# Kernel tuning notes

Measured on AMD Instinct MI355X. Metric: run time of the kernel, lower is better.

Reference implementation:

```python
import jax, jax.numpy as jnp
import numpy as np

B, T, H = 4, 4096, 2048
NUM_HEADS, HEAD_DIM = 16, 128


def setup_inputs() -> dict:
    key = jax.random.key(0)
    k1, k2, k3 = jax.random.split(key, 3)
    hidden = jax.random.normal(k1, (B, T, H), dtype=jnp.float32)
    # Linear(H -> 3H): store weight as [H, 3H] for x @ W
    w_qkv = jax.random.normal(k2, (H, 3 * H), dtype=jnp.float32) * (1.0 / np.sqrt(H))
    b_qkv = jax.random.normal(k3, (3 * H,), dtype=jnp.float32) * 0.02
    return {"hidden": hidden, "w_qkv": w_qkv, "b_qkv": b_qkv}


def _to_heads(x):
    # (B, T, H) -> (B, num_heads, T, head_dim)
    b, t, _ = x.shape
    return x.reshape(b, t, NUM_HEADS, HEAD_DIM).transpose(0, 2, 1, 3)


def reference(hidden, w_qkv, b_qkv):
    # fused QKV projection: (B,T,H) @ (H,3H) + (3H,)
    qkv = jnp.einsum('bth,hd->btd', hidden, w_qkv) + b_qkv
    q, k, v = jnp.split(qkv, 3, axis=-1)
    return _to_heads(q), _to_heads(k), _to_heads(v)
```

## Files before the change

### kernel.cpp

```cpp
#include <hip/hip_runtime.h>
#include <hip/hip_bf16.h>
#include <stdint.h>

#define M_DIM 16384
#define K_DIM 2048
#define N_DIM 6144
#define NT    32
#define NTILES 6

typedef __attribute__((ext_vector_type(8))) short bf16x8;
typedef __attribute__((ext_vector_type(8))) unsigned short u16x8;
typedef __attribute__((ext_vector_type(4))) float f32x4;

__device__ __forceinline__ unsigned short f2bf(float f) {
  unsigned int u = __float_as_uint(f);
  u += 0x7FFFu + ((u >> 16) & 1u);
  return (unsigned short)(u >> 16);
}

__device__ __forceinline__ void load_lds16(const void* g, void* l) {
  __builtin_amdgcn_global_load_lds((const __attribute__((address_space(1))) void*)g,
                                   (__attribute__((address_space(3))) void*)l, 16, 0, 0);
}

#define FENCE asm volatile("" ::: "memory")
#define BAR   do { FENCE; __builtin_amdgcn_s_barrier(); FENCE; } while (0)
#define LGKM0 do { asm volatile("s_waitcnt lgkmcnt(0)" ::: "memory"); \
                   __builtin_amdgcn_sched_barrier(0); } while (0)

__global__ __launch_bounds__(256) void cvt_hidden(const float* __restrict__ in,
                                                  unsigned short* __restrict__ out) {
  unsigned int base = blockIdx.x * 256u + threadIdx.x;
  #pragma unroll
  for (int i = 0; i < 16; ++i) {
    unsigned int fi = i * 524288u + base;
    float4 v = reinterpret_cast<const float4*>(in)[fi];
    ushort4 o;
    o.x = f2bf(v.x); o.y = f2bf(v.y); o.z = f2bf(v.z); o.w = f2bf(v.w);
    reinterpret_cast<ushort4*>(out)[fi] = o;
  }
}

__global__ __launch_bounds__(256) void cvt_w(const float* __restrict__ w,
                                             unsigned short* __restrict__ wt) {
  __shared__ float tile[64][69];
  const int k0 = blockIdx.x * 64;
  const int n0 = blockIdx.y * 64;
  const int t = threadIdx.x;
  #pragma unroll
  for (int i = 0; i < 4; ++i) {
    int idx = i * 256 + t;
    int row = idx >> 4, c4 = idx & 15;
    float4 v = *reinterpret_cast<const float4*>(&w[(size_t)(k0 + row) * N_DIM + n0 + c4 * 4]);
    tile[row][c4 * 4 + 0] = v.x; tile[row][c4 * 4 + 1] = v.y;
    tile[row][c4 * 4 + 2] = v.z; tile[row][c4 * 4 + 3] = v.w;
  }
  __syncthreads();
  #pragma unroll
  for (int i = 0; i < 2; ++i) {
    int idx = i * 256 + t;
    int n = idx >> 3, k8 = idx & 7;
    u16x8 v;
    #pragma unroll
    for (int e = 0; e < 8; ++e) v[e] = f2bf(tile[k8 * 8 + e][n]);
    *reinterpret_cast<u16x8*>(&wt[(size_t)(n0 + n) * K_DIM + k0 + k8 * 8]) = v;
  }
}

__global__ __launch_bounds__(512, 2) void gemm_qkv_8ph(const unsigned short* __restrict__ A,
                                                       const unsigned short* __restrict__ Bt,
                                                       const float* __restrict__ bias,
                                                       float* __restrict__ out) {
  extern __shared__ __align__(16) char smem[];
  const int tid = threadIdx.x, lane = tid & 63, wid = tid >> 6;
  const int wm = wid >> 2, wn = wid & 3;

  const int xcd = blockIdx.x & 7;
  const int lcl = blockIdx.x >> 3;

  const int srow  = tid >> 3;
  const int sslot = (tid & 7) ^ ((tid >> 3) & 7);
  const int r15 = lane & 15, q4 = lane >> 4, x7 = lane & 7;
  const int abase = (wm * 128 + r15) * 128;
  const int bbase = (wn * 64  + r15) * 128;
  const int sw0 = ((0 + q4) ^ x7) * 16;
  const int sw1 = ((4 + q4) ^ x7) * 16;

  #define STAGE_T(gsrc, ldsbase)                                              \
    { const unsigned short* _g = (gsrc); char* _l = (ldsbase);                \
      load_lds16(_g,                       _l +     wid * 1024);              \
      load_lds16(_g + (size_t)64  * K_DIM, _l + 8192  + wid * 1024);          \
      load_lds16(_g + (size_t)128 * K_DIM, _l + 16384 + wid * 1024);          \
      load_lds16(_g + (size_t)192 * K_DIM, _l + 24576 + wid * 1024); }

  #define TILE_PARAMS(j, m0_, n0_, gA_, gB_)                                  \
    { const int idx = (j) * 32 + lcl;                                         \
      const int bm = xcd * 8 + idx / 24, bn = idx % 24;                       \
      m0_ = bm * 256; n0_ = bn * 256;                                         \
      gA_ = A  + (size_t)(m0_ + srow) * K_DIM + sslot * 8;                    \
      gB_ = Bt + (size_t)(n0_ + srow) * K_DIM + sslot * 8; }

  char* A0 = smem;          char* B0 = smem + 32768;
  char* A1 = smem + 65536;  char* B1 = smem + 98304;

  int m0, n0;
  const unsigned short *gA, *gB;
  TILE_PARAMS(0, m0, n0, gA, gB);
  STAGE_T(gB +  0, B0); STAGE_T(gA +  0, A0);
  STAGE_T(gB + 64, B1); STAGE_T(gA + 64, A1);
  asm volatile("s_waitcnt vmcnt(8)" ::: "memory");
  BAR;

  for (int j = 0; j < NTILES; ++j) {
    float4 bv4[2][2];
    #pragma unroll
    for (int qn = 0; qn < 2; ++qn)
      #pragma unroll
      for (int ni = 0; ni < 2; ++ni)
        bv4[qn][ni] = *reinterpret_cast<const float4*>(
            &bias[n0 + wn * 64 + qn * 32 + ni * 16 + q4 * 4]);

    f32x4 acc[2][2][4][2] = {};
    bf16x8 a[4][2], b0[2][2], b1[2][2];

    for (int t = 0; t < NT; ++t) {
      char* Ab = smem + (t & 1) * 65536;
      char* Bb = Ab + 32768;
      const bool st = (t + 2 < NT);

      #pragma unroll
      for (int mi = 0; mi < 4; ++mi) {
        const char* p = Ab + abase + mi * (16 * 128);
        a[mi][0] = *(const bf16x8*)(p + sw0);
        a[mi][1] = *(const bf16x8*)(p + sw1);
      }
      #pragma unroll
      for (int ni = 0; ni < 2; ++ni) {
        const char* p = Bb + bbase + ni * (16 * 128);
        b0[ni][0] = *(const bf16x8*)(p + sw0);
        b0[ni][1] = *(const bf16x8*)(p + sw1);
      }
      BAR; LGKM0;
      __builtin_amdgcn_s_setprio(1);
      #pragma unroll
      for (int mi = 0; mi < 4; ++mi)
        #pragma unroll
        for (int ni = 0; ni < 2; ++ni) {
          acc[0][0][mi][ni] = __builtin_amdgcn_mfma_f32_16x16x32_bf16(b0[ni][0], a[mi][0], acc[0][0][mi][ni], 0, 0, 0);
          acc[0][0][mi][ni] = __builtin_amdgcn_mfma_f32_16x16x32_bf16(b0[ni][1], a[mi][1], acc[0][0][mi][ni], 0, 0, 0);
        }
      __builtin_amdgcn_s_setprio(0);
      BAR;

      #pragma unroll
      for (int ni = 0; ni < 2; ++ni) {
        const char* p = Bb + bbase + (32 + ni * 16) * 128;
        b1[ni][0] = *(const bf16x8*)(p + sw0);
        b1[ni][1] = *(const bf16x8*)(p + sw1);
      }
      BAR; LGKM0;
      __builtin_amdgcn_s_setprio(1);
      #pragma unroll
      for (int mi = 0; mi < 4; ++mi)
        #pragma unroll
        for (int ni = 0; ni < 2; ++ni) {
          acc[0][1][mi][ni] = __builtin_amdgcn_mfma_f32_16x16x32_bf16(b1[ni][0], a[mi][0], acc[0][1][mi][ni], 0, 0, 0);
          acc[0][1][mi][ni] = __builtin_amdgcn_mfma_f32_16x16x32_bf16(b1[ni][1], a[mi][1], acc[0][1][mi][ni], 0, 0, 0);
        }
      __builtin_amdgcn_s_setprio(0);
      BAR;

      #pragma unroll
      for (int mi = 0; mi < 4; ++mi) {
        const char* p = Ab + abase + (64 + mi * 16) * 128;
        a[mi][0] = *(const bf16x8*)(p + sw0);
        a[mi][1] = *(const bf16x8*)(p + sw1);
      }
      if (st) STAGE_T(gB + (size_t)(t + 2) * 64, Bb);
      BAR; LGKM0;
      __builtin_amdgcn_s_setprio(1);
      #pragma unroll
      for (int mi = 0; mi < 4; ++mi)
        #pragma unroll
        for (int ni = 0; ni < 2; ++ni) {
          acc[1][0][mi][ni] = __builtin_amdgcn_mfma_f32_16x16x32_bf16(b0[ni][0], a[mi][0], acc[1][0][mi][ni], 0, 0, 0);
          acc[1][0][mi][ni] = __builtin_amdgcn_mfma_f32_16x16x32_bf16(b0[ni][1], a[mi][1], acc[1][0][mi][ni], 0, 0, 0);
        }
      __builtin_amdgcn_s_setprio(0);
      BAR;

      if (st) STAGE_T(gA + (size_t)(t + 2) * 64, Ab);
      BAR; LGKM0;
      __builtin_amdgcn_s_setprio(1);
      #pragma unroll
      for (int mi = 0; mi < 4; ++mi)
        #pragma unroll
        for (int ni = 0; ni < 2; ++ni) {
          acc[1][1][mi][ni] = __builtin_amdgcn_mfma_f32_16x16x32_bf16(b1[ni][0], a[mi][0], acc[1][1][mi][ni], 0, 0, 0);
          acc[1][1][mi][ni] = __builtin_amdgcn_mfma_f32_16x16x32_bf16(b1[ni][1], a[mi][1], acc[1][1][mi][ni], 0, 0, 0);
        }
      __builtin_amdgcn_s_setprio(0);
      if (st) { asm volatile("s_waitcnt vmcnt(8)" ::: "memory"); }
      else    { asm volatile("s_waitcnt vmcnt(0)" ::: "memory"); }
      BAR;
    }

    const int cm0 = m0, cn0 = n0;
    if (j + 1 < NTILES) {
      TILE_PARAMS(j + 1, m0, n0, gA, gB);
      STAGE_T(gB +  0, B0); STAGE_T(gA +  0, A0);
      STAGE_T(gB + 64, B1); STAGE_T(gA + 64, A1);
    }

    #pragma unroll
    for (int qm = 0; qm < 2; ++qm)
      #pragma unroll
      for (int mi = 0; mi < 4; ++mi) {
        const int m = cm0 + wm * 128 + qm * 64 + mi * 16 + r15;
        const int bb_ = m >> 12, tt = m & 4095;
        float* orow = out + (size_t)bb_ * 8388608 + (size_t)tt * 128;
        #pragma unroll
        for (int qn = 0; qn < 2; ++qn)
          #pragma unroll
          for (int ni = 0; ni < 2; ++ni) {
            const int col = cn0 + wn * 64 + qn * 32 + ni * 16 + q4 * 4;
            const int which = col >> 11, head = (col & 2047) >> 7, hd = col & 127;
            float4 v;
            v.x = acc[qm][qn][mi][ni][0] + bv4[qn][ni].x;
            v.y = acc[qm][qn][mi][ni][1] + bv4[qn][ni].y;
            v.z = acc[qm][qn][mi][ni][2] + bv4[qn][ni].z;
            v.w = acc[qm][qn][mi][ni][3] + bv4[qn][ni].w;
            *reinterpret_cast<float4*>(orow + (size_t)which * 33554432 +
                                       (size_t)head * 524288 + hd) = v;
          }
      }

    if (j + 1 < NTILES) {
      asm volatile("s_waitcnt vmcnt(40)" ::: "memory");
      BAR;
    }
  }
  #undef STAGE_T
  #undef TILE_PARAMS
}

__global__ __launch_bounds__(256) void naive_qkv(const float* __restrict__ h,
                                                 const float* __restrict__ w,
                                                 const float* __restrict__ bias,
                                                 float* __restrict__ out) {
  const int m = blockIdx.x;
  const int n = blockIdx.y * 256 + threadIdx.x;
  const float* hr = h + (size_t)m * K_DIM;
  float acc = bias[n];
  for (int k = 0; k < K_DIM; ++k) acc = fmaf(hr[k], w[(size_t)k * N_DIM + n], acc);
  const int which = n >> 11, head = (n & 2047) >> 7, hd = n & 127;
  const int bb = m >> 12, tt = m & 4095;
  out[(size_t)which * 33554432 + (size_t)bb * 8388608 + (size_t)head * 524288 +
      (size_t)tt * 128 + hd] = acc;
}

extern "C" void kernel_launch(void* const* d_in, const int* in_sizes, int n_in,
                              void* d_out, int out_size, void* d_ws, size_t ws_size,
                              hipStream_t stream) {
  const float* hidden = (const float*)d_in[0];
  const float* w_qkv  = (const float*)d_in[1];
  const float* b_qkv  = (const float*)d_in[2];
  float* out = (float*)d_out;

  const size_t needA = (size_t)M_DIM * K_DIM * 2;
  const size_t needB = (size_t)N_DIM * K_DIM * 2;
  if (ws_size >= needA + needB) {
    unsigned short* Abf = (unsigned short*)d_ws;
    unsigned short* Wt  = (unsigned short*)((char*)d_ws + needA);
    (void)hipFuncSetAttribute((const void*)gemm_qkv_8ph,
                              hipFuncAttributeMaxDynamicSharedMemorySize, 131072);
    cvt_hidden<<<2048, 256, 0, stream>>>(hidden, Abf);
    cvt_w<<<dim3(32, 96), 256, 0, stream>>>(w_qkv, Wt);
    gemm_qkv_8ph<<<256, 512, 131072, stream>>>(Abf, Wt, b_qkv, out);
  } else {
    naive_qkv<<<dim3(16384, 24), 256, 0, stream>>>(hidden, w_qkv, b_qkv, out);
  }
}
```

Measured before the change: 479.7 us.

## Pipeline next tile's K-prefetch across tile boundary and remap tiles per CTA

```diff
diff --git a/kernel.cpp b/kernel.cpp
--- a/kernel.cpp
+++ b/kernel.cpp
@@ -93,32 +93,37 @@
       load_lds16(_g + (size_t)128 * K_DIM, _l + 16384 + wid * 1024);          \
       load_lds16(_g + (size_t)192 * K_DIM, _l + 24576 + wid * 1024); }
 
-  #define TILE_PARAMS(j, m0_, n0_, gA_, gB_)                                  \
-    { const int idx = (j) * 32 + lcl;                                         \
-      const int bm = xcd * 8 + idx / 24, bn = idx % 24;                       \
-      m0_ = bm * 256; n0_ = bn * 256;                                         \
+  #define TILE_MAP(jj, m0_, n0_, gA_, gB_)                                    \
+    { const int bm_ = xcd * 8 + (lcl >> 2);                                   \
+      const int bn_ = (jj) * 4 + (lcl & 3);                                   \
+      m0_ = bm_ * 256; n0_ = bn_ * 256;                                       \
       gA_ = A  + (size_t)(m0_ + srow) * K_DIM + sslot * 8;                    \
       gB_ = Bt + (size_t)(n0_ + srow) * K_DIM + sslot * 8; }
 
-  char* A0 = smem;          char* B0 = smem + 32768;
-  char* A1 = smem + 65536;  char* B1 = smem + 98304;
-
-  int m0, n0;
-  const unsigned short *gA, *gB;
-  TILE_PARAMS(0, m0, n0, gA, gB);
-  STAGE_T(gB +  0, B0); STAGE_T(gA +  0, A0);
-  STAGE_T(gB + 64, B1); STAGE_T(gA + 64, A1);
-  asm volatile("s_waitcnt vmcnt(8)" ::: "memory");
-  BAR;
+  if (tid < 384) {
+    const int jj = tid / 64;
+    const int o  = (tid & 63) * 4;
+    const int bn_ = jj * 4 + (lcl & 3);
+    float4 bv = *reinterpret_cast<const float4*>(&bias[bn_ * 256 + o]);
+    *reinterpret_cast<float4*>(smem + 131072 + jj * 1024 + o * 4) = bv;
+  }
+  __builtin_amdgcn_sched_barrier(0);
+
+  int m0, n0, m0n, n0n;
+  const unsigned short *gA, *gB, *gAn, *gBn;
+  TILE_MAP(0, m0, n0, gA, gB);
+  {
+    char* A0 = smem;          char* B0 = smem + 32768;
+    char* A1 = smem + 65536;  char* B1 = smem + 98304;
+    STAGE_T(gB +  0, B0); STAGE_T(gA +  0, A0);
+    STAGE_T(gB + 64, B1); STAGE_T(gA + 64, A1);
+    asm volatile("s_waitcnt vmcnt(8)" ::: "memory");
+    BAR;
+  }
 
   for (int j = 0; j < NTILES; ++j) {
-    float4 bv4[2][2];
-    #pragma unroll
-    for (int qn = 0; qn < 2; ++qn)
-      #pragma unroll
-      for (int ni = 0; ni < 2; ++ni)
-        bv4[qn][ni] = *reinterpret_cast<const float4*>(
-            &bias[n0 + wn * 64 + qn * 32 + ni * 16 + q4 * 4]);
+    const int jn = (j + 1 < NTILES) ? j + 1 : j;
+    TILE_MAP(jn, m0n, n0n, gAn, gBn);
 
     f32x4 acc[2][2][4][2] = {};
     bf16x8 a[4][2], b0[2][2], b1[2][2];
@@ -126,7 +131,11 @@
     for (int t = 0; t < NT; ++t) {
       char* Ab = smem + (t & 1) * 65536;
       char* Bb = Ab + 32768;
-      const bool st = (t + 2 < NT);
+      const bool st = (t + 2 < NT) || (j + 1 < NTILES);
+      const unsigned short* sA = (t + 2 < NT) ? gA + (size_t)(t + 2) * 64
+                                              : gAn + (size_t)(t + 2 - NT) * 64;
+      const unsigned short* sB = (t + 2 < NT) ? gB + (size_t)(t + 2) * 64
+                                              : gBn + (size_t)(t + 2 - NT) * 64;
 
       #pragma unroll
       for (int mi = 0; mi < 4; ++mi) {
@@ -176,7 +185,7 @@
         a[mi][0] = *(const bf16x8*)(p + sw0);
         a[mi][1] = *(const bf16x8*)(p + sw1);
       }
-      if (st) STAGE_T(gB + (size_t)(t + 2) * 64, Bb);
+      if (st) STAGE_T(sB, Bb);
       BAR; LGKM0;
       __builtin_amdgcn_s_setprio(1);
       #pragma unroll
@@ -189,7 +198,7 @@
       __builtin_amdgcn_s_setprio(0);
       BAR;
 
-      if (st) STAGE_T(gA + (size_t)(t + 2) * 64, Ab);
+      if (st) STAGE_T(sA, Ab);
       BAR; LGKM0;
       __builtin_amdgcn_s_setprio(1);
       #pragma unroll
@@ -200,48 +209,48 @@
           acc[1][1][mi][ni] = __builtin_amdgcn_mfma_f32_16x16x32_bf16(b1[ni][1], a[mi][1], acc[1][1][mi][ni], 0, 0, 0);
         }
       __builtin_amdgcn_s_setprio(0);
-      if (st) { asm volatile("s_waitcnt vmcnt(8)" ::: "memory"); }
-      else    { asm volatile("s_waitcnt vmcnt(0)" ::: "memory"); }
+      if (t == 0 && j != 0)  { asm volatile("s_waitcnt vmcnt(40)" ::: "memory"); }
+      else if (st)           { asm volatile("s_waitcnt vmcnt(8)"  ::: "memory"); }
+      else                   { asm volatile("s_waitcnt vmcnt(0)"  ::: "memory"); }
       BAR;
     }
 
-    const int cm0 = m0, cn0 = n0;
-    if (j + 1 < NTILES) {
-      TILE_PARAMS(j + 1, m0, n0, gA, gB);
-      STAGE_T(gB +  0, B0); STAGE_T(gA +  0, A0);
-      STAGE_T(gB + 64, B1); STAGE_T(gA + 64, A1);
-    }
+    const char* bl = smem + 131072 + j * 1024;
+    float4 bq[2][2];
+    #pragma unroll
+    for (int qn = 0; qn < 2; ++qn)
+      #pragma unroll
+      for (int ni = 0; ni < 2; ++ni)
+        bq[qn][ni] = *reinterpret_cast<const float4*>(
+            bl + (wn * 64 + qn * 32 + ni * 16 + q4 * 4) * 4);
 
     #pragma unroll
     for (int qm = 0; qm < 2; ++qm)
       #pragma unroll
       for (int mi = 0; mi < 4; ++mi) {
-        const int m = cm0 + wm * 128 + qm * 64 + mi * 16 + r15;
+        const int m = m0 + wm * 128 + qm * 64 + mi * 16 + r15;
         const int bb_ = m >> 12, tt = m & 4095;
         float* orow = out + (size_t)bb_ * 8388608 + (size_t)tt * 128;
         #pragma unroll
         for (int qn = 0; qn < 2; ++qn)
           #pragma unroll
           for (int ni = 0; ni < 2; ++ni) {
-            const int col = cn0 + wn * 64 + qn * 32 + ni * 16 + q4 * 4;
+            const int col = n0 + wn * 64 + qn * 32 + ni * 16 + q4 * 4;
             const int which = col >> 11, head = (col & 2047) >> 7, hd = col & 127;
             float4 v;
-            v.x = acc[qm][qn][mi][ni][0] + bv4[qn][ni].x;
-            v.y = acc[qm][qn][mi][ni][1] + bv4[qn][ni].y;
-            v.z = acc[qm][qn][mi][ni][2] + bv4[qn][ni].z;
-            v.w = acc[qm][qn][mi][ni][3] + bv4[qn][ni].w;
+            v.x = acc[qm][qn][mi][ni][0] + bq[qn][ni].x;
+            v.y = acc[qm][qn][mi][ni][1] + bq[qn][ni].y;
+            v.z = acc[qm][qn][mi][ni][2] + bq[qn][ni].z;
+            v.w = acc[qm][qn][mi][ni][3] + bq[qn][ni].w;
             *reinterpret_cast<float4*>(orow + (size_t)which * 33554432 +
                                        (size_t)head * 524288 + hd) = v;
           }
       }
 
-    if (j + 1 < NTILES) {
-      asm volatile("s_waitcnt vmcnt(40)" ::: "memory");
-      BAR;
-    }
+    m0 = m0n; n0 = n0n; gA = gAn; gB = gBn;
   }
   #undef STAGE_T
-  #undef TILE_PARAMS
+  #undef TILE_MAP
 }
 
 __global__ __launch_bounds__(256) void naive_qkv(const float* __restrict__ h,
@@ -273,10 +282,10 @@
     unsigned short* Abf = (unsigned short*)d_ws;
     unsigned short* Wt  = (unsigned short*)((char*)d_ws + needA);
     (void)hipFuncSetAttribute((const void*)gemm_qkv_8ph,
-                              hipFuncAttributeMaxDynamicSharedMemorySize, 131072);
+                              hipFuncAttributeMaxDynamicSharedMemorySize, 137216);
     cvt_hidden<<<2048, 256, 0, stream>>>(hidden, Abf);
     cvt_w<<<dim3(32, 96), 256, 0, stream>>>(w_qkv, Wt);
-    gemm_qkv_8ph<<<256, 512, 131072, stream>>>(Abf, Wt, b_qkv, out);
+    gemm_qkv_8ph<<<256, 512, 137216, stream>>>(Abf, Wt, b_qkv, out);
   } else {
     naive_qkv<<<dim3(16384, 24), 256, 0, stream>>>(hidden, w_qkv, b_qkv, out);
   }
```

Result: no change. 484.3 us (+1.0%).
